# Kernel optimization log

Hardware: AMD Instinct MI355X
Metric: run time of the kernel (lower is better)

## Reference

```python
import jax, jax.numpy as jnp
import numpy as np

B, T, K = 256, 512, 4
VC, VS = 8000, 20000
DC, DS = 128, 128
H = 256
L = 32


def setup_inputs() -> dict:
    key = jax.random.key(0)
    ks = jax.random.split(key, 16)
    s = lambda k, shape, sc: jax.random.normal(k, shape, jnp.float32) * sc
    D = DC + DS
    return {
        "char_ids": jax.random.randint(ks[0], (B, T), 0, VC),
        "sense_ids": jax.random.randint(ks[1], (B, T, K), 0, VS),
        "mask": jnp.ones((B, T), dtype=bool),
        "labels": jax.random.randint(ks[2], (B, T), 0, L),
        "E_char": s(ks[3], (VC, DC), 0.1),
        "E_sense": s(ks[4], (VS, DS), 0.1),
        "Wih_f": s(ks[5], (4 * H, D), 0.05),
        "Whh_f": s(ks[6], (4 * H, H), 0.05),
        "b_f": jnp.zeros((4 * H,), jnp.float32),
        "Wih_b": s(ks[7], (4 * H, D), 0.05),
        "Whh_b": s(ks[8], (4 * H, H), 0.05),
        "b_b": jnp.zeros((4 * H,), jnp.float32),
        "W_proj": s(ks[9], (2 * H, L), 0.05),
        "b_proj": jnp.zeros((L,), jnp.float32),
        "trans": s(ks[10], (L, L), 0.1),
        "start_trans": s(ks[11], (L,), 0.1),
        "end_trans": s(ks[12], (L,), 0.1),
    }


def _lstm(x, Wih, Whh, b):
    # x: [T,B,D] -> hidden states [T,B,H]; torch gate order i,f,g,o
    Hd = Whh.shape[1]
    Bn = x.shape[1]

    def step(carry, xt):
        h, c = carry
        z = xt @ Wih.T + h @ Whh.T + b  # [B,4H]
        i, f, g, o = jnp.split(z, 4, axis=-1)
        c = jax.nn.sigmoid(f) * c + jax.nn.sigmoid(i) * jnp.tanh(g)
        h = jax.nn.sigmoid(o) * jnp.tanh(c)
        return (h, c), h

    h0 = jnp.zeros((Bn, Hd), x.dtype)
    _, hs = jax.lax.scan(step, (h0, h0), x)
    return hs


def _crf_nll(emissions, tags, mask, trans, start_trans, end_trans):
    # emissions [T,B,L], tags [T,B] int, mask [T,B] float (mask[0]==1)
    Bn = emissions.shape[1]
    bidx = jnp.arange(Bn)
    # ---- numerator: score of gold path ----
    score0 = start_trans[tags[0]] + emissions[0, bidx, tags[0]]

    def num_step(carry, inps):
        score, prev = carry
        em_t, tag_t, m_t = inps
        step = trans[prev, tag_t] + em_t[bidx, tag_t]
        score = score + step * m_t
        prev = jnp.where(m_t.astype(bool), tag_t, prev)
        return (score, prev), None

    (score, last_tag), _ = jax.lax.scan(
        num_step, (score0, tags[0]), (emissions[1:], tags[1:], mask[1:]))
    score = score + end_trans[last_tag]
    # ---- partition function (forward algorithm) ----
    alpha0 = start_trans + emissions[0]  # [B,L]

    def part_step(alpha, inps):
        em_t, m_t = inps
        nxt = jax.scipy.special.logsumexp(
            alpha[:, :, None] + trans[None], axis=1) + em_t
        alpha = jnp.where(m_t[:, None].astype(bool), nxt, alpha)
        return alpha, None

    alpha, _ = jax.lax.scan(part_step, alpha0, (emissions[1:], mask[1:]))
    logZ = jax.scipy.special.logsumexp(alpha + end_trans, axis=1)
    llh = score - logZ  # [B]
    # pytorch-crf reduction='token_mean'; model returns loss = -llh_mean
    return -(llh.sum() / mask.sum())


def reference(char_ids, sense_ids, mask, labels, E_char, E_sense,
              Wih_f, Whh_f, b_f, Wih_b, Whh_b, b_b,
              W_proj, b_proj, trans, start_trans, end_trans):
    # embedding: char vector + mean-pooled lexicon-sense vectors
    emb = jnp.concatenate(
        [E_char[char_ids], E_sense[sense_ids].mean(axis=2)], axis=-1)  # [B,T,D]
    x = emb.transpose(1, 0, 2)  # [T,B,D]
    hf = _lstm(x, Wih_f, Whh_f, b_f)
    hb = _lstm(x[::-1], Wih_b, Whh_b, b_b)[::-1]
    h = jnp.concatenate([hf, hb], axis=-1)  # [T,B,2H]
    emissions = h @ W_proj + b_proj  # [T,B,L]
    m = mask.T.astype(emissions.dtype)
    return _crf_nll(emissions, labels.T, m, trans, start_trans, end_trans)
```

## Files before the change

### kernel.cpp

```cpp
#include <hip/hip_runtime.h>


typedef unsigned int  uint_t;
typedef unsigned short ushort_t;
typedef __attribute__((ext_vector_type(8))) short  v8s;
typedef __attribute__((ext_vector_type(4))) float  v4f;
typedef __attribute__((ext_vector_type(4))) uint_t v4u;

#define T_LEN 512
#define B_SZ  256
#define D_IN  256
#define SENT  0x7F807F80u

__device__ inline ushort_t f2bf(float f) {
  uint_t u = __float_as_uint(f);
  u = (u + 0x7fffu + ((u >> 16) & 1u)) >> 16;
  return (ushort_t)u;
}
__device__ inline float sigmoidf_(float x) { return 1.f / (1.f + __expf(-x)); }
__device__ inline float tanhf_(float x) {
  x = fminf(fmaxf(x, -15.f), 15.f);
  float e = __expf(-2.f * x);
  return (1.f - e) / (1.f + e);
}

__global__ void embed_kernel(const int* __restrict__ char_ids,
                             const int* __restrict__ sense_ids,
                             const float* __restrict__ E_char,
                             const float* __restrict__ E_sense,
                             ushort_t* __restrict__ xb) {
  int tk = blockIdx.x * 4 + (threadIdx.x >> 6);
  int lane = threadIdx.x & 63;
  int t = tk >> 8, b = tk & 255;
  ushort_t* dst = xb + (size_t)tk * D_IN;
  if (lane < 32) {
    int cid = char_ids[b * T_LEN + t];
    float4 v = *reinterpret_cast<const float4*>(E_char + (size_t)cid * 128 + lane * 4);
    ushort4 o; o.x = f2bf(v.x); o.y = f2bf(v.y); o.z = f2bf(v.z); o.w = f2bf(v.w);
    *reinterpret_cast<ushort4*>(dst + lane * 4) = o;
  } else {
    int l2 = lane - 32;
    const int* sp = sense_ids + ((size_t)b * T_LEN + t) * 4;
    float ax = 0, ay = 0, az = 0, aw = 0;
#pragma unroll
    for (int k = 0; k < 4; ++k) {
      float4 v = *reinterpret_cast<const float4*>(E_sense + (size_t)sp[k] * 128 + l2 * 4);
      ax += v.x; ay += v.y; az += v.z; aw += v.w;
    }
    ushort4 o; o.x = f2bf(ax * .25f); o.y = f2bf(ay * .25f);
    o.z = f2bf(az * .25f); o.w = f2bf(aw * .25f);
    *reinterpret_cast<ushort4*>(dst + 128 + l2 * 4) = o;
  }
}

__global__ void prefill_kernel(uint_t* __restrict__ p) {
  v4u s4 = {SENT, SENT, SENT, SENT};
  size_t i = (size_t)blockIdx.x * 256 + threadIdx.x;
  uint_t* base = p + i * 4;
#pragma unroll
  for (int q = 0; q < 4; ++q) {
    uint_t* a = base + (size_t)q * 8388608;
    asm volatile("global_store_dwordx4 %0, %1, off sc0 sc1"
                 :: "v"(a), "v"(s4) : "memory");
  }
}

__global__ void repack_w_kernel(const float* __restrict__ Wih_f, const float* __restrict__ Whh_f,
                                const float* __restrict__ Wih_b, const float* __restrict__ Whh_b,
                                ushort_t* __restrict__ Wcat) {
  int w = blockIdx.x;
  int R = w & 1023;
  int orig = (R & 3) * 256 + (R >> 7) * 32 + ((R & 127) >> 2);
  const float* ih = (w >> 10) ? Wih_b : Wih_f;
  const float* hh = (w >> 10) ? Whh_b : Whh_f;
  ushort_t* dst = Wcat + (size_t)w * 512;
#pragma unroll
  for (int i = 0; i < 2; ++i) {
    int k = threadIdx.x + 256 * i;
    float v = (k < 256) ? ih[orig * 256 + k] : hh[orig * 256 + (k - 256)];
    dst[k] = f2bf(v);
  }
}

__global__ void repack_misc_kernel(const float* __restrict__ b_f, const float* __restrict__ b_b,
                                   const float* __restrict__ W_proj,
                                   float* __restrict__ bcat, ushort_t* __restrict__ Wpt) {
  int tid = threadIdx.x;
  for (int e = tid; e < 2048; e += 256) {
    int R = e & 1023;
    int orig = (R & 3) * 256 + (R >> 7) * 32 + ((R & 127) >> 2);
    bcat[e] = (e >> 10) ? b_b[orig] : b_f[orig];
  }
  for (int e = tid; e < 32 * 512; e += 256) {
    int l = e >> 9, k = e & 511;
    Wpt[e] = f2bf(W_proj[k * 32 + l]);
  }
}


#define PINW(W) asm volatile("" : "+v"(W[0]), "+v"(W[1]), "+v"(W[2]),          \
                                  "+v"(W[3]), "+v"(W[4]), "+v"(W[5]),          \
                                  "+v"(W[6]), "+v"(W[7]))

__global__ __launch_bounds__(256, 1) __attribute__((amdgpu_waves_per_eu(1, 1)))
void lstm_kernel(const ushort_t* __restrict__ xb,
                 ushort_t* __restrict__ hf, ushort_t* __restrict__ hb,
                 const ushort_t* __restrict__ Wcat, const float* __restrict__ bcat) {
  __shared__ __align__(16) ushort_t lds_hq[8 * 512];
  __shared__ __align__(16) ushort_t lds_h[4 * 128];
  const int tid = threadIdx.x;
  const int wg = blockIdx.x;
  const int cl = wg & 15;
  const int dir = (wg >> 4) & 1;
  const int s = wg >> 5;
  const int bg = cl * 16;
  const int wave = tid >> 6, lane = tid & 63;
  const int n = lane & 15;
  const int ko = 8 * (lane >> 4);
  const int rowb = s * 128 + wave * 32;

  const ushort_t* wrow0 = Wcat + ((size_t)(dir * 1024 + rowb + n)) * 512;
  const ushort_t* wrow1 = wrow0 + 16 * 512;
  v8s wx0[8], wh0[8], wx1[8], wh1[8];
#pragma unroll
  for (int kk = 0; kk < 8; ++kk) {
    wx0[kk] = *reinterpret_cast<const v8s*>(wrow0 + kk * 32 + ko);
    wh0[kk] = *reinterpret_cast<const v8s*>(wrow0 + 256 + kk * 32 + ko);
    wx1[kk] = *reinterpret_cast<const v8s*>(wrow1 + kk * 32 + ko);
    wh1[kk] = *reinterpret_cast<const v8s*>(wrow1 + 256 + kk * 32 + ko);
  }
  PINW(wx0); PINW(wh0); PINW(wx1); PINW(wh1);
  const float4 b40 = *reinterpret_cast<const float4*>(
      bcat + dir * 1024 + rowb + (lane >> 4) * 4);
  const float4 b41 = *reinterpret_cast<const float4*>(
      bcat + dir * 1024 + rowb + 16 + (lane >> 4) * 4);
  ushort_t* hbuf = dir ? hb : hf;

  v4u xv[8];
  {
    const int t0 = dir ? (T_LEN - 1) : 0;
    const v4u* xr = reinterpret_cast<const v4u*>(
        xb + ((size_t)t0 * B_SZ + bg + n) * D_IN + ko);
#pragma unroll
    for (int kk = 0; kk < 8; ++kk) xv[kk] = xr[kk * 4];
  }
  float c0 = 0.f, c1 = 0.f;

#pragma unroll 1
  for (int step = 0; step < T_LEN; ++step) {
    const int t = dir ? (T_LEN - 1 - step) : step;
    v8s hv[8];
    if (step > 0) {
      const int tp = dir ? (t + 1) : (t - 1);
      const ushort_t* base = hbuf + (((size_t)tp * 8) * B_SZ + bg + n) * 32 + ko;
      const ushort_t* pA = base + (size_t)(2 * wave) * B_SZ * 32;
      const ushort_t* pB = base + (size_t)(2 * wave + 1) * B_SZ * 32;
      v4u qA, qB;
      for (;;) {
        asm volatile(
            "global_load_dwordx4 %0, %2, off sc0 sc1\n\t"
            "global_load_dwordx4 %1, %3, off sc0 sc1\n\t"
            "s_waitcnt vmcnt(0)"
            : "=&v"(qA), "=&v"(qB) : "v"(pA), "v"(pB));
        uint_t ok = (uint_t)(qA[0] != SENT) & (uint_t)(qA[1] != SENT) &
                    (uint_t)(qA[2] != SENT) & (uint_t)(qA[3] != SENT) &
                    (uint_t)(qB[0] != SENT) & (uint_t)(qB[1] != SENT) &
                    (uint_t)(qB[2] != SENT) & (uint_t)(qB[3] != SENT);
        if (__all((int)ok)) break;
        __builtin_amdgcn_s_sleep(1);
      }
      {
        ushort_t* lw = lds_hq + (2 * wave) * 512 + (lane >> 4) * 128 + n * 8;
        *reinterpret_cast<v4u*>(lw) = qA;
        *reinterpret_cast<v4u*>(lw + 512) = qB;
      }
      __syncthreads();
      const ushort_t* lr = lds_hq + (lane >> 4) * 128 + n * 8;
#pragma unroll
      for (int kk = 0; kk < 8; ++kk)
        hv[kk] = *reinterpret_cast<const v8s*>(lr + kk * 512);
    }
    v4f a0 = {0.f, 0.f, 0.f, 0.f}, a1 = {0.f, 0.f, 0.f, 0.f};
#pragma unroll
    for (int kk = 0; kk < 8; ++kk) {
      union { v4u u; v8s v; } cx; cx.u = xv[kk];
      a0 = __builtin_amdgcn_mfma_f32_16x16x32_bf16(wx0[kk], cx.v, a0, 0, 0, 0);
      a1 = __builtin_amdgcn_mfma_f32_16x16x32_bf16(wx1[kk], cx.v, a1, 0, 0, 0);
    }
    if (step > 0) {
#pragma unroll
      for (int kk = 0; kk < 8; ++kk) {
        a0 = __builtin_amdgcn_mfma_f32_16x16x32_bf16(wh0[kk], hv[kk], a0, 0, 0, 0);
        a1 = __builtin_amdgcn_mfma_f32_16x16x32_bf16(wh1[kk], hv[kk], a1, 0, 0, 0);
      }
    }
    {
      float zi = a0[0] + b40.x, zf = a0[1] + b40.y;
      float zg = a0[2] + b40.z, zo = a0[3] + b40.w;
      c0 = sigmoidf_(zf) * c0 + sigmoidf_(zi) * tanhf_(zg);
      lds_h[wave * 128 + n * 8 + (lane >> 4)] = f2bf(sigmoidf_(zo) * tanhf_(c0));
    }
    {
      float zi = a1[0] + b41.x, zf = a1[1] + b41.y;
      float zg = a1[2] + b41.z, zo = a1[3] + b41.w;
      c1 = sigmoidf_(zf) * c1 + sigmoidf_(zi) * tanhf_(zg);
      lds_h[wave * 128 + n * 8 + 4 + (lane >> 4)] = f2bf(sigmoidf_(zo) * tanhf_(c1));
    }
    if (lane < 16) {
      v8s hv16 = ((const v8s*)lds_h)[wave * 16 + lane];
      ushort_t* dst = hbuf + (((size_t)t * 8 + s) * B_SZ + bg + lane) * 32 + wave * 8;
      asm volatile("global_store_dwordx4 %0, %1, off sc0 sc1"
                   :: "v"(dst), "v"(hv16));
    }
    if (step < T_LEN - 1) {
      const int tn = dir ? (t - 1) : (t + 1);
      const v4u* xr = reinterpret_cast<const v4u*>(
          xb + ((size_t)tn * B_SZ + bg + n) * D_IN + ko);
#pragma unroll
      for (int kk = 0; kk < 8; ++kk) xv[kk] = xr[kk * 4];
    }
  }
}

__global__ __launch_bounds__(256)
void emis_kernel(const ushort_t* __restrict__ hf, const ushort_t* __restrict__ hb,
                 const ushort_t* __restrict__ Wpt, const float* __restrict__ bproj,
                 float* __restrict__ em) {
  __shared__ char wsm[32 * 1024];
  int tid = threadIdx.x;
#pragma unroll
  for (int i = 0; i < 8; ++i) {
    int cc = tid + 256 * i;
    int row = cc >> 6, kc = cc & 63;
    v8s v = *reinterpret_cast<const v8s*>(Wpt + row * 512 + kc * 8);
    *reinterpret_cast<v8s*>(wsm + row * 1024 + ((kc * 16) ^ ((row & 7) << 4))) = v;
  }
  __syncthreads();
  int wave = tid >> 6, lane = tid & 63;
  int t = blockIdx.x;
  int ko = 8 * (lane >> 4);
  int r0 = lane & 15;
  int wr0 = (lane & 15), wr1 = (lane & 15) + 16;
  int wb0 = wr0 * 1024, wx0 = (wr0 & 7) << 4;
  int wb1 = wr1 * 1024, wx1 = (wr1 & 7) << 4;
  v4f acc[4][2];
#pragma unroll
  for (int m = 0; m < 4; ++m) { acc[m][0] = (v4f){0, 0, 0, 0}; acc[m][1] = (v4f){0, 0, 0, 0}; }
#pragma unroll
  for (int kk = 0; kk < 8; ++kk) {
    int k2 = (kk * 32 + ko) * 2;
    v8s b0 = *reinterpret_cast<const v8s*>(wsm + wb0 + (k2 ^ wx0));
    v8s b1 = *reinterpret_cast<const v8s*>(wsm + wb1 + (k2 ^ wx1));
#pragma unroll
    for (int m = 0; m < 4; ++m) {
      int b = wave * 64 + m * 16 + r0;
      v8s a = *reinterpret_cast<const v8s*>(
          hf + (((size_t)t * 8 + kk) * B_SZ + b) * 32 + ko);
      acc[m][0] = __builtin_amdgcn_mfma_f32_16x16x32_bf16(a, b0, acc[m][0], 0, 0, 0);
      acc[m][1] = __builtin_amdgcn_mfma_f32_16x16x32_bf16(a, b1, acc[m][1], 0, 0, 0);
    }
  }
#pragma unroll
  for (int kk = 0; kk < 8; ++kk) {
    int k2 = (256 + kk * 32 + ko) * 2;
    v8s b0 = *reinterpret_cast<const v8s*>(wsm + wb0 + (k2 ^ wx0));
    v8s b1 = *reinterpret_cast<const v8s*>(wsm + wb1 + (k2 ^ wx1));
#pragma unroll
    for (int m = 0; m < 4; ++m) {
      int b = wave * 64 + m * 16 + r0;
      v8s a = *reinterpret_cast<const v8s*>(
          hb + (((size_t)t * 8 + kk) * B_SZ + b) * 32 + ko);
      acc[m][0] = __builtin_amdgcn_mfma_f32_16x16x32_bf16(a, b0, acc[m][0], 0, 0, 0);
      acc[m][1] = __builtin_amdgcn_mfma_f32_16x16x32_bf16(a, b1, acc[m][1], 0, 0, 0);
    }
  }
  float bp0 = bproj[lane & 15], bp1 = bproj[16 + (lane & 15)];
#pragma unroll
  for (int m = 0; m < 4; ++m)
#pragma unroll
    for (int r = 0; r < 4; ++r) {
      int tok = t * 256 + wave * 64 + m * 16 + (lane >> 4) * 4 + r;
      em[(size_t)tok * 32 + (lane & 15)] = acc[m][0][r] + bp0;
      em[(size_t)tok * 32 + 16 + (lane & 15)] = acc[m][1][r] + bp1;
    }
}

__global__ __launch_bounds__(256)
void crf_kernel(const float* __restrict__ em, const int* __restrict__ labels,
                const float* __restrict__ trans, const float* __restrict__ strans,
                const float* __restrict__ etrans, float* __restrict__ llh) {
  int tid = threadIdx.x;
  int widx = blockIdx.x * 4 + (tid >> 6);
  int lane = tid & 63;
  int half = lane >> 5, j = lane & 31;
  int b = widx * 2 + half;
  const int* lab = labels + (size_t)b * T_LEN;

  float sc = 0.f;
  {
    int t0 = j * 16 + 1;
    int prev = lab[t0 - 1];
    for (int t = t0; t < t0 + 16 && t < T_LEN; ++t) {
      int tg = lab[t];
      sc += trans[prev * 32 + tg] + em[((size_t)t * B_SZ + b) * 32 + tg];
      prev = tg;
    }
#pragma unroll
    for (int m = 16; m; m >>= 1) sc += __shfl_xor(sc, m, 32);
  }
  int tg0 = lab[0], tgL = lab[T_LEN - 1];
  float score = sc + strans[tg0] + em[(size_t)b * 32 + tg0] + etrans[tgL];

  float P[32];
#pragma unroll
  for (int i = 0; i < 32; ++i) P[i] = __expf(trans[i * 32 + j]);
  float alpha0 = strans[j] + em[(size_t)b * 32 + j];
  float M = alpha0;
#pragma unroll
  for (int d = 16; d; d >>= 1) M = fmaxf(M, __shfl_xor(M, d, 32));
  float A = __expf(alpha0 - M);

  for (int tb = 1; tb < T_LEN; tb += 8) {
    float eq[8];
#pragma unroll
    for (int q = 0; q < 8; ++q) {
      int t = tb + q;
      eq[q] = (t < T_LEN) ? em[((size_t)t * B_SZ + b) * 32 + j] : 0.f;
    }
#pragma unroll
    for (int q = 0; q < 8; ++q) {
      int t = tb + q;
      if (t >= T_LEN) break;
      float ssum = 0.f;
#pragma unroll
      for (int i = 0; i < 32; ++i) ssum += __shfl(A, (half << 5) + i, 64) * P[i];
      A = ssum * __expf(eq[q]);
    }
    float m = A;
#pragma unroll
    for (int d = 16; d; d >>= 1) m = fmaxf(m, __shfl_xor(m, d, 32));
    M += __logf(m);
    A /= m;
  }
  float v = A * __expf(etrans[j]);
  float s2 = v;
#pragma unroll
  for (int d = 16; d; d >>= 1) s2 += __shfl_xor(s2, d, 32);
  if (j == 0) llh[b] = score - (M + __logf(s2));
}

__global__ void fin_kernel(const float* __restrict__ llh, float* __restrict__ out) {
  __shared__ float red[256];
  int tid = threadIdx.x;
  red[tid] = llh[tid];
  __syncthreads();
  for (int s = 128; s; s >>= 1) {
    if (tid < s) red[tid] += red[tid + s];
    __syncthreads();
  }
  if (tid == 0) out[0] = -red[0] / 131072.0f;
}

extern "C" void kernel_launch(void* const* d_in, const int* in_sizes, int n_in,
                              void* d_out, int out_size, void* d_ws, size_t ws_size,
                              hipStream_t stream) {
  const int* char_ids = (const int*)d_in[0];
  const int* sense_ids = (const int*)d_in[1];
  const int* labels = (const int*)d_in[3];
  const float* E_char = (const float*)d_in[4];
  const float* E_sense = (const float*)d_in[5];
  const float* Wih_f = (const float*)d_in[6];
  const float* Whh_f = (const float*)d_in[7];
  const float* b_f = (const float*)d_in[8];
  const float* Wih_b = (const float*)d_in[9];
  const float* Whh_b = (const float*)d_in[10];
  const float* b_b = (const float*)d_in[11];
  const float* W_proj = (const float*)d_in[12];
  const float* b_proj = (const float*)d_in[13];
  const float* trans = (const float*)d_in[14];
  const float* strans = (const float*)d_in[15];
  const float* etrans = (const float*)d_in[16];
  float* out = (float*)d_out;

  char* ws = (char*)d_ws;
  ushort_t* xb   = (ushort_t*)(ws + 0);
  ushort_t* hf   = (ushort_t*)(ws + 67108864);
  ushort_t* hb   = (ushort_t*)(ws + 134217728);
  float*    em   = (float*)(ws + 201326592);
  ushort_t* Wcat = (ushort_t*)(ws + 218103808);
  float*    bcat = (float*)(ws + 220200960);
  ushort_t* Wpt  = (ushort_t*)(ws + 220209152);
  float*    llh  = (float*)(ws + 220241920);

  repack_w_kernel<<<2048, 256, 0, stream>>>(Wih_f, Whh_f, Wih_b, Whh_b, Wcat);
  repack_misc_kernel<<<1, 256, 0, stream>>>(b_f, b_b, W_proj, bcat, Wpt);
  embed_kernel<<<(T_LEN * B_SZ) / 4, 256, 0, stream>>>(char_ids, sense_ids, E_char, E_sense, xb);
  prefill_kernel<<<8192, 256, 0, stream>>>((uint_t*)(ws + 67108864));
  lstm_kernel<<<256, 256, 0, stream>>>(xb, hf, hb, Wcat, bcat);
  emis_kernel<<<T_LEN, 256, 0, stream>>>(hf, hb, Wpt, b_proj, em);
  crf_kernel<<<32, 256, 0, stream>>>(em, labels, trans, strans, etrans, llh);
  fin_kernel<<<1, 256, 0, stream>>>(llh, out);
}
```

Baseline: 1.596 ms.

## Stage LSTM weight slices in swizzled LDS instead of pinning them in registers

The persistent LSTM kernel now copies each workgroup's 128x512 bf16 weight slice into 128 KB of dynamic shared memory with an XOR swizzle, and reads the MFMA A-operands from LDS every step instead of keeping them pinned in VGPRs. The aim is to cut register pressure (and drop the waves_per_eu pin), giving the compiler room to schedule the recurrent loop. In exchange each step now does 32 extra LDS reads per wave on the latency-critical recurrence path, and a second __syncthreads is added to protect the h staging buffer.

```diff
diff --git a/kernel.cpp b/kernel.cpp
--- a/kernel.cpp
+++ b/kernel.cpp
@@ -98,16 +98,13 @@
 }
 
 
-#define PINW(W) asm volatile("" : "+v"(W[0]), "+v"(W[1]), "+v"(W[2]),          \
-                                  "+v"(W[3]), "+v"(W[4]), "+v"(W[5]),          \
-                                  "+v"(W[6]), "+v"(W[7]))
-
-__global__ __launch_bounds__(256, 1) __attribute__((amdgpu_waves_per_eu(1, 1)))
+__global__ __launch_bounds__(256, 1)
 void lstm_kernel(const ushort_t* __restrict__ xb,
                  ushort_t* __restrict__ hf, ushort_t* __restrict__ hb,
                  const ushort_t* __restrict__ Wcat, const float* __restrict__ bcat) {
-  __shared__ __align__(16) ushort_t lds_hq[8 * 512];
-  __shared__ __align__(16) ushort_t lds_h[4 * 128];
+  extern __shared__ char smem[];
+  ushort_t* lds_hq = (ushort_t*)(smem + 131072);
+  ushort_t* lds_ht = (ushort_t*)(smem + 131072 + 8192);
   const int tid = threadIdx.x;
   const int wg = blockIdx.x;
   const int cl = wg & 15;
@@ -117,24 +114,27 @@
   const int wave = tid >> 6, lane = tid & 63;
   const int n = lane & 15;
   const int ko = 8 * (lane >> 4);
+
+  {
+    const ushort_t* wsrc = Wcat + (size_t)(dir * 1024 + s * 128) * 512;
+#pragma unroll
+    for (int i = 0; i < 32; ++i) {
+      int cc = tid + 256 * i;
+      int row = cc >> 6, kc = cc & 63;
+      v8s v = *reinterpret_cast<const v8s*>(wsrc + row * 512 + kc * 8);
+      *reinterpret_cast<v8s*>(smem + row * 1024 + ((kc * 16) ^ ((row & 7) << 4))) = v;
+    }
+  }
   const int rowb = s * 128 + wave * 32;
-
-  const ushort_t* wrow0 = Wcat + ((size_t)(dir * 1024 + rowb + n)) * 512;
-  const ushort_t* wrow1 = wrow0 + 16 * 512;
-  v8s wx0[8], wh0[8], wx1[8], wh1[8];
-#pragma unroll
-  for (int kk = 0; kk < 8; ++kk) {
-    wx0[kk] = *reinterpret_cast<const v8s*>(wrow0 + kk * 32 + ko);
-    wh0[kk] = *reinterpret_cast<const v8s*>(wrow0 + 256 + kk * 32 + ko);
-    wx1[kk] = *reinterpret_cast<const v8s*>(wrow1 + kk * 32 + ko);
-    wh1[kk] = *reinterpret_cast<const v8s*>(wrow1 + 256 + kk * 32 + ko);
-  }
-  PINW(wx0); PINW(wh0); PINW(wx1); PINW(wh1);
   const float4 b40 = *reinterpret_cast<const float4*>(
       bcat + dir * 1024 + rowb + (lane >> 4) * 4);
   const float4 b41 = *reinterpret_cast<const float4*>(
       bcat + dir * 1024 + rowb + 16 + (lane >> 4) * 4);
   ushort_t* hbuf = dir ? hb : hf;
+  const int wb0 = (wave * 32 + n) * 1024;
+  const int wb1 = wb0 + 16 * 1024;
+  const int wxr = (n & 7) << 4;
+  __syncthreads();
 
   v4u xv[8];
   {
@@ -179,35 +179,42 @@
 #pragma unroll
       for (int kk = 0; kk < 8; ++kk)
         hv[kk] = *reinterpret_cast<const v8s*>(lr + kk * 512);
+      __syncthreads();
     }
     v4f a0 = {0.f, 0.f, 0.f, 0.f}, a1 = {0.f, 0.f, 0.f, 0.f};
 #pragma unroll
     for (int kk = 0; kk < 8; ++kk) {
+      int k2 = (kk * 32 + ko) * 2;
+      v8s w0 = *reinterpret_cast<const v8s*>(smem + wb0 + (k2 ^ wxr));
+      v8s w1 = *reinterpret_cast<const v8s*>(smem + wb1 + (k2 ^ wxr));
       union { v4u u; v8s v; } cx; cx.u = xv[kk];
-      a0 = __builtin_amdgcn_mfma_f32_16x16x32_bf16(wx0[kk], cx.v, a0, 0, 0, 0);
-      a1 = __builtin_amdgcn_mfma_f32_16x16x32_bf16(wx1[kk], cx.v, a1, 0, 0, 0);
+      a0 = __builtin_amdgcn_mfma_f32_16x16x32_bf16(w0, cx.v, a0, 0, 0, 0);
+      a1 = __builtin_amdgcn_mfma_f32_16x16x32_bf16(w1, cx.v, a1, 0, 0, 0);
     }
     if (step > 0) {
 #pragma unroll
       for (int kk = 0; kk < 8; ++kk) {
-        a0 = __builtin_amdgcn_mfma_f32_16x16x32_bf16(wh0[kk], hv[kk], a0, 0, 0, 0);
-        a1 = __builtin_amdgcn_mfma_f32_16x16x32_bf16(wh1[kk], hv[kk], a1, 0, 0, 0);
+        int k2 = 512 + (kk * 32 + ko) * 2;
+        v8s w0 = *reinterpret_cast<const v8s*>(smem + wb0 + (k2 ^ wxr));
+        v8s w1 = *reinterpret_cast<const v8s*>(smem + wb1 + (k2 ^ wxr));
+        a0 = __builtin_amdgcn_mfma_f32_16x16x32_bf16(w0, hv[kk], a0, 0, 0, 0);
+        a1 = __builtin_amdgcn_mfma_f32_16x16x32_bf16(w1, hv[kk], a1, 0, 0, 0);
       }
     }
     {
       float zi = a0[0] + b40.x, zf = a0[1] + b40.y;
       float zg = a0[2] + b40.z, zo = a0[3] + b40.w;
       c0 = sigmoidf_(zf) * c0 + sigmoidf_(zi) * tanhf_(zg);
-      lds_h[wave * 128 + n * 8 + (lane >> 4)] = f2bf(sigmoidf_(zo) * tanhf_(c0));
+      lds_ht[wave * 128 + n * 8 + (lane >> 4)] = f2bf(sigmoidf_(zo) * tanhf_(c0));
     }
     {
       float zi = a1[0] + b41.x, zf = a1[1] + b41.y;
       float zg = a1[2] + b41.z, zo = a1[3] + b41.w;
       c1 = sigmoidf_(zf) * c1 + sigmoidf_(zi) * tanhf_(zg);
-      lds_h[wave * 128 + n * 8 + 4 + (lane >> 4)] = f2bf(sigmoidf_(zo) * tanhf_(c1));
+      lds_ht[wave * 128 + n * 8 + 4 + (lane >> 4)] = f2bf(sigmoidf_(zo) * tanhf_(c1));
     }
     if (lane < 16) {
-      v8s hv16 = ((const v8s*)lds_h)[wave * 16 + lane];
+      v8s hv16 = ((const v8s*)lds_ht)[wave * 16 + lane];
       ushort_t* dst = hbuf + (((size_t)t * 8 + s) * B_SZ + bg + lane) * 32 + wave * 8;
       asm volatile("global_store_dwordx4 %0, %1, off sc0 sc1"
                    :: "v"(dst), "v"(hv16));
@@ -392,11 +399,15 @@
   ushort_t* Wpt  = (ushort_t*)(ws + 220209152);
   float*    llh  = (float*)(ws + 220241920);
 
+  static const int lstm_lds = 131072 + 8192 + 1024;
+  hipFuncSetAttribute((const void*)lstm_kernel,
+                      hipFuncAttributeMaxDynamicSharedMemorySize, lstm_lds);
+
   repack_w_kernel<<<2048, 256, 0, stream>>>(Wih_f, Whh_f, Wih_b, Whh_b, Wcat);
   repack_misc_kernel<<<1, 256, 0, stream>>>(b_f, b_b, W_proj, bcat, Wpt);
   embed_kernel<<<(T_LEN * B_SZ) / 4, 256, 0, stream>>>(char_ids, sense_ids, E_char, E_sense, xb);
   prefill_kernel<<<8192, 256, 0, stream>>>((uint_t*)(ws + 67108864));
-  lstm_kernel<<<256, 256, 0, stream>>>(xb, hf, hb, Wcat, bcat);
+  lstm_kernel<<<256, 256, lstm_lds, stream>>>(xb, hf, hb, Wcat, bcat);
   emis_kernel<<<T_LEN, 256, 0, stream>>>(hf, hb, Wpt, b_proj, em);
   crf_kernel<<<32, 256, 0, stream>>>(em, labels, trans, strans, etrans, llh);
   fin_kernel<<<1, 256, 0, stream>>>(llh, out);
```

New measurement: 1.737 ms. 1.09x slower.

## Rewrite LSTM hidden-state spin-wait in asm with double-buffered LDS and early x prefetch

Applied to the files above, without the earlier changes.

The sentinel polling loop on the previous step's hidden state moves into inline assembly: dword loads, scalar-mask compares and a branch, replacing the vector compare plus __all reduction. The LDS exchange buffer becomes double-buffered by step parity, which may cut a barrier hazard between consecutive steps. The next timestep's x loads now issue before the MFMA work into separate registers instead of after the store. This shortens the per-step latency on the serial recurrence, at the cost of extra registers and extra LDS.

```diff
diff --git a/kernel.cpp b/kernel.cpp
--- a/kernel.cpp
+++ b/kernel.cpp
@@ -3,6 +3,7 @@
 
 typedef unsigned int  uint_t;
 typedef unsigned short ushort_t;
+typedef unsigned long long u64_t;
 typedef __attribute__((ext_vector_type(8))) short  v8s;
 typedef __attribute__((ext_vector_type(4))) float  v4f;
 typedef __attribute__((ext_vector_type(4))) uint_t v4u;
@@ -106,8 +107,8 @@
 void lstm_kernel(const ushort_t* __restrict__ xb,
                  ushort_t* __restrict__ hf, ushort_t* __restrict__ hb,
                  const ushort_t* __restrict__ Wcat, const float* __restrict__ bcat) {
-  __shared__ __align__(16) ushort_t lds_hq[8 * 512];
-  __shared__ __align__(16) ushort_t lds_h[4 * 128];
+  __shared__ __align__(16) ushort_t lds_hq[2][8 * 512];
+  __shared__ __align__(16) ushort_t lds_ht[4 * 128];
   const int tid = threadIdx.x;
   const int wg = blockIdx.x;
   const int cl = wg & 15;
@@ -149,75 +150,109 @@
 #pragma unroll 1
   for (int step = 0; step < T_LEN; ++step) {
     const int t = dir ? (T_LEN - 1 - step) : step;
+    const int par = step & 1;
     v8s hv[8];
+    uint_t a0, a1, a2, a3, b0, b1, b2, b3;
     if (step > 0) {
       const int tp = dir ? (t + 1) : (t - 1);
       const ushort_t* base = hbuf + (((size_t)tp * 8) * B_SZ + bg + n) * 32 + ko;
       const ushort_t* pA = base + (size_t)(2 * wave) * B_SZ * 32;
       const ushort_t* pB = base + (size_t)(2 * wave + 1) * B_SZ * 32;
-      v4u qA, qB;
-      for (;;) {
-        asm volatile(
-            "global_load_dwordx4 %0, %2, off sc0 sc1\n\t"
-            "global_load_dwordx4 %1, %3, off sc0 sc1\n\t"
-            "s_waitcnt vmcnt(0)"
-            : "=&v"(qA), "=&v"(qB) : "v"(pA), "v"(pB));
-        uint_t ok = (uint_t)(qA[0] != SENT) & (uint_t)(qA[1] != SENT) &
-                    (uint_t)(qA[2] != SENT) & (uint_t)(qA[3] != SENT) &
-                    (uint_t)(qB[0] != SENT) & (uint_t)(qB[1] != SENT) &
-                    (uint_t)(qB[2] != SENT) & (uint_t)(qB[3] != SENT);
-        if (__all((int)ok)) break;
-        __builtin_amdgcn_s_sleep(1);
-      }
-      {
-        ushort_t* lw = lds_hq + (2 * wave) * 512 + (lane >> 4) * 128 + n * 8;
-        *reinterpret_cast<v4u*>(lw) = qA;
-        *reinterpret_cast<v4u*>(lw + 512) = qB;
-      }
-      __syncthreads();
-      const ushort_t* lr = lds_hq + (lane >> 4) * 128 + n * 8;
-#pragma unroll
-      for (int kk = 0; kk < 8; ++kk)
-        hv[kk] = *reinterpret_cast<const v8s*>(lr + kk * 512);
-    }
-    v4f a0 = {0.f, 0.f, 0.f, 0.f}, a1 = {0.f, 0.f, 0.f, 0.f};
-#pragma unroll
-    for (int kk = 0; kk < 8; ++kk) {
-      union { v4u u; v8s v; } cx; cx.u = xv[kk];
-      a0 = __builtin_amdgcn_mfma_f32_16x16x32_bf16(wx0[kk], cx.v, a0, 0, 0, 0);
-      a1 = __builtin_amdgcn_mfma_f32_16x16x32_bf16(wx1[kk], cx.v, a1, 0, 0, 0);
-    }
-    if (step > 0) {
-#pragma unroll
-      for (int kk = 0; kk < 8; ++kk) {
-        a0 = __builtin_amdgcn_mfma_f32_16x16x32_bf16(wh0[kk], hv[kk], a0, 0, 0, 0);
-        a1 = __builtin_amdgcn_mfma_f32_16x16x32_bf16(wh1[kk], hv[kk], a1, 0, 0, 0);
-      }
-    }
-    {
-      float zi = a0[0] + b40.x, zf = a0[1] + b40.y;
-      float zg = a0[2] + b40.z, zo = a0[3] + b40.w;
-      c0 = sigmoidf_(zf) * c0 + sigmoidf_(zi) * tanhf_(zg);
-      lds_h[wave * 128 + n * 8 + (lane >> 4)] = f2bf(sigmoidf_(zo) * tanhf_(c0));
-    }
-    {
-      float zi = a1[0] + b41.x, zf = a1[1] + b41.y;
-      float zg = a1[2] + b41.z, zo = a1[3] + b41.w;
-      c1 = sigmoidf_(zf) * c1 + sigmoidf_(zi) * tanhf_(zg);
-      lds_h[wave * 128 + n * 8 + 4 + (lane >> 4)] = f2bf(sigmoidf_(zo) * tanhf_(c1));
-    }
-    if (lane < 16) {
-      v8s hv16 = ((const v8s*)lds_h)[wave * 16 + lane];
-      ushort_t* dst = hbuf + (((size_t)t * 8 + s) * B_SZ + bg + lane) * 32 + wave * 8;
-      asm volatile("global_store_dwordx4 %0, %1, off sc0 sc1"
-                   :: "v"(dst), "v"(hv16));
-    }
+      u64_t m_;
+      asm volatile(
+          "2:\n\t"
+          "global_load_dword %[a0], %[pa], off sc0 sc1\n\t"
+          "global_load_dword %[a1], %[pa], off offset:4 sc0 sc1\n\t"
+          "global_load_dword %[a2], %[pa], off offset:8 sc0 sc1\n\t"
+          "global_load_dword %[a3], %[pa], off offset:12 sc0 sc1\n\t"
+          "global_load_dword %[b0], %[pb], off sc0 sc1\n\t"
+          "global_load_dword %[b1], %[pb], off offset:4 sc0 sc1\n\t"
+          "global_load_dword %[b2], %[pb], off offset:8 sc0 sc1\n\t"
+          "global_load_dword %[b3], %[pb], off offset:12 sc0 sc1\n\t"
+          "s_waitcnt vmcnt(0)\n\t"
+          "v_cmp_ne_u32 vcc, 0x7f807f80, %[a0]\n\t"
+          "s_and_b64 %[m], vcc, exec\n\t"
+          "v_cmp_ne_u32 vcc, 0x7f807f80, %[a1]\n\t"
+          "s_and_b64 %[m], %[m], vcc\n\t"
+          "v_cmp_ne_u32 vcc, 0x7f807f80, %[a2]\n\t"
+          "s_and_b64 %[m], %[m], vcc\n\t"
+          "v_cmp_ne_u32 vcc, 0x7f807f80, %[a3]\n\t"
+          "s_and_b64 %[m], %[m], vcc\n\t"
+          "v_cmp_ne_u32 vcc, 0x7f807f80, %[b0]\n\t"
+          "s_and_b64 %[m], %[m], vcc\n\t"
+          "v_cmp_ne_u32 vcc, 0x7f807f80, %[b1]\n\t"
+          "s_and_b64 %[m], %[m], vcc\n\t"
+          "v_cmp_ne_u32 vcc, 0x7f807f80, %[b2]\n\t"
+          "s_and_b64 %[m], %[m], vcc\n\t"
+          "v_cmp_ne_u32 vcc, 0x7f807f80, %[b3]\n\t"
+          "s_and_b64 %[m], %[m], vcc\n\t"
+          "s_andn2_b64 %[m], exec, %[m]\n\t"
+          "s_cbranch_scc0 3f\n\t"
+          "s_sleep 1\n\t"
+          "s_branch 2b\n\t"
+          "3:"
+          : [a0] "=&v"(a0), [a1] "=&v"(a1), [a2] "=&v"(a2), [a3] "=&v"(a3),
+            [b0] "=&v"(b0), [b1] "=&v"(b1), [b2] "=&v"(b2), [b3] "=&v"(b3),
+            [m] "=&s"(m_)
+          : [pa] "v"(pA), [pb] "v"(pB)
+          : "vcc");
+      __builtin_amdgcn_sched_barrier(0);
+    }
+    v4u xn[8];
     if (step < T_LEN - 1) {
       const int tn = dir ? (t - 1) : (t + 1);
       const v4u* xr = reinterpret_cast<const v4u*>(
           xb + ((size_t)tn * B_SZ + bg + n) * D_IN + ko);
 #pragma unroll
-      for (int kk = 0; kk < 8; ++kk) xv[kk] = xr[kk * 4];
+      for (int kk = 0; kk < 8; ++kk) xn[kk] = xr[kk * 4];
+    }
+    if (step > 0) {
+      ushort_t* lw = &lds_hq[par][(2 * wave) * 512 + (lane >> 4) * 128 + n * 8];
+      uint_t* lwa = (uint_t*)lw;
+      lwa[0] = a0; lwa[1] = a1; lwa[2] = a2; lwa[3] = a3;
+      uint_t* lwb = (uint_t*)(lw + 512);
+      lwb[0] = b0; lwb[1] = b1; lwb[2] = b2; lwb[3] = b3;
+      __syncthreads();
+      const ushort_t* lr = &lds_hq[par][(lane >> 4) * 128 + n * 8];
+#pragma unroll
+      for (int kk = 0; kk < 8; ++kk)
+        hv[kk] = *reinterpret_cast<const v8s*>(lr + kk * 512);
+    }
+    v4f a0f = {0.f, 0.f, 0.f, 0.f}, a1f = {0.f, 0.f, 0.f, 0.f};
+#pragma unroll
+    for (int kk = 0; kk < 8; ++kk) {
+      union { v4u u; v8s v; } cx; cx.u = xv[kk];
+      a0f = __builtin_amdgcn_mfma_f32_16x16x32_bf16(wx0[kk], cx.v, a0f, 0, 0, 0);
+      a1f = __builtin_amdgcn_mfma_f32_16x16x32_bf16(wx1[kk], cx.v, a1f, 0, 0, 0);
+    }
+    if (step > 0) {
+#pragma unroll
+      for (int kk = 0; kk < 8; ++kk) {
+        a0f = __builtin_amdgcn_mfma_f32_16x16x32_bf16(wh0[kk], hv[kk], a0f, 0, 0, 0);
+        a1f = __builtin_amdgcn_mfma_f32_16x16x32_bf16(wh1[kk], hv[kk], a1f, 0, 0, 0);
+      }
+    }
+    {
+      float zi = a0f[0] + b40.x, zf = a0f[1] + b40.y;
+      float zg = a0f[2] + b40.z, zo = a0f[3] + b40.w;
+      c0 = sigmoidf_(zf) * c0 + sigmoidf_(zi) * tanhf_(zg);
+      lds_ht[wave * 128 + n * 8 + (lane >> 4)] = f2bf(sigmoidf_(zo) * tanhf_(c0));
+    }
+    {
+      float zi = a1f[0] + b41.x, zf = a1f[1] + b41.y;
+      float zg = a1f[2] + b41.z, zo = a1f[3] + b41.w;
+      c1 = sigmoidf_(zf) * c1 + sigmoidf_(zi) * tanhf_(zg);
+      lds_ht[wave * 128 + n * 8 + 4 + (lane >> 4)] = f2bf(sigmoidf_(zo) * tanhf_(c1));
+    }
+    if (lane < 16) {
+      v8s hv16 = ((const v8s*)lds_ht)[wave * 16 + lane];
+      ushort_t* dst = hbuf + (((size_t)t * 8 + s) * B_SZ + bg + lane) * 32 + wave * 8;
+      asm volatile("global_store_dwordx4 %0, %1, off sc0 sc1"
+                   :: "v"(dst), "v"(hv16));
+    }
+    if (step < T_LEN - 1) {
+#pragma unroll
+      for (int kk = 0; kk < 8; ++kk) xv[kk] = xn[kk];
     }
   }
 }
```

After: 3.501 ms. 2.19x slower.
